# Performance work log

Hardware: AMD Instinct MI355X
Metric: run time of the kernel (lower is better)

Reference implementation:

```python
import jax, jax.numpy as jnp
import numpy as np

LN_EPS = 1e-6

def _ln_proj(x, ln_scale, ln_bias, kernel, bias):
    # LayerNorm over last dim, then GEMM projection. Dropout is identity
    # (deterministic / eval mode, training=False default).
    mu = jnp.mean(x, axis=-1, keepdims=True)
    var = jnp.mean(jnp.square(x - mu), axis=-1, keepdims=True)
    xn = (x - mu) * jax.lax.rsqrt(var + LN_EPS) * ln_scale + ln_bias
    return jnp.einsum('bsh,hp->bsp', xn, kernel) + bias


def setup_inputs() -> dict:
    key = jax.random.key(0)
    ks = jax.random.split(key, 4)
    B, S, H, P = 2, 4096, 4096, 1024
    return {
        'vision_features': jax.random.normal(ks[0], (B, S, H), dtype=jnp.float32),
        'text_features': jax.random.normal(ks[1], (B, S, H), dtype=jnp.float32),
        'v_ln_scale': jnp.ones((H,), jnp.float32),
        'v_ln_bias': jnp.zeros((H,), jnp.float32),
        'v_kernel': jax.random.normal(ks[2], (H, P), dtype=jnp.float32) / np.sqrt(H).astype(np.float32),
        'v_bias': jnp.zeros((P,), jnp.float32),
        't_ln_scale': jnp.ones((H,), jnp.float32),
        't_ln_bias': jnp.zeros((H,), jnp.float32),
        't_kernel': jax.random.normal(ks[3], (H, P), dtype=jnp.float32) / np.sqrt(H).astype(np.float32),
        't_bias': jnp.zeros((P,), jnp.float32),
    }


def reference(vision_features, text_features, v_ln_scale, v_ln_bias, v_kernel, v_bias,
              t_ln_scale, t_ln_bias, t_kernel, t_bias):
    vision_projected = _ln_proj(vision_features, v_ln_scale, v_ln_bias, v_kernel, v_bias)
    text_projected = _ln_proj(text_features, t_ln_scale, t_ln_bias, t_kernel, t_bias)
    return (vision_projected, text_projected)
```

## Files before the change

### kernel.cpp

```cpp
#include <hip/hip_runtime.h>
#include <hip/hip_bf16.h>
#include <stdint.h>

#define LN_EPS 1e-6f

typedef __bf16 bf16x8 __attribute__((ext_vector_type(8)));
typedef float f32x4 __attribute__((ext_vector_type(4)));

__device__ __forceinline__ unsigned short f2bf(float f) {
    uint32_t u = __float_as_uint(f);
    uint32_t r = (u + 0x7fffu + ((u >> 16) & 1u)) >> 16;
    return (unsigned short)r;
}

__device__ __forceinline__ void async_copy16(const void* g, void* l) {
    const __attribute__((address_space(1))) uint32_t* gp =
        (const __attribute__((address_space(1))) uint32_t*)(uintptr_t)g;
    __attribute__((address_space(3))) uint32_t* lp =
        (__attribute__((address_space(3))) uint32_t*)(uint32_t)(uintptr_t)l;
    __builtin_amdgcn_global_load_lds(gp, lp, 16, 0, 0);
}

__global__ __launch_bounds__(256) void ln_bf16_kernel(
    const float* __restrict__ x0, const float* __restrict__ x1,
    const float* __restrict__ s0, const float* __restrict__ b0,
    const float* __restrict__ s1, const float* __restrict__ b1,
    unsigned short* __restrict__ y0, unsigned short* __restrict__ y1, int H)
{
    int row = blockIdx.x;
    int prob = blockIdx.y;
    const float* x = (prob ? x1 : x0) + (size_t)row * H;
    const float* s = prob ? s1 : s0;
    const float* b = prob ? b1 : b0;
    unsigned short* y = (prob ? y1 : y0) + (size_t)row * H;
    int t = threadIdx.x;

    float4 v[4];
    float sum = 0.f, sq = 0.f;
#pragma unroll
    for (int g = 0; g < 4; ++g) {
        v[g] = ((const float4*)x)[t + 256 * g];
        sum += v[g].x + v[g].y + v[g].z + v[g].w;
        sq  += v[g].x * v[g].x + v[g].y * v[g].y + v[g].z * v[g].z + v[g].w * v[g].w;
    }
#pragma unroll
    for (int off = 32; off > 0; off >>= 1) {
        sum += __shfl_xor(sum, off, 64);
        sq  += __shfl_xor(sq, off, 64);
    }
    __shared__ float ssum[4], ssq[4];
    int wave = t >> 6;
    if ((t & 63) == 0) { ssum[wave] = sum; ssq[wave] = sq; }
    __syncthreads();
    sum = ssum[0] + ssum[1] + ssum[2] + ssum[3];
    sq  = ssq[0] + ssq[1] + ssq[2] + ssq[3];
    float mu = sum * (1.0f / 4096.0f);
    float var = sq * (1.0f / 4096.0f) - mu * mu;
    float rstd = rsqrtf(var + LN_EPS);

#pragma unroll
    for (int g = 0; g < 4; ++g) {
        int i4 = t + 256 * g;
        float4 sc = ((const float4*)s)[i4];
        float4 bi = ((const float4*)b)[i4];
        ushort4 o;
        o.x = f2bf((v[g].x - mu) * rstd * sc.x + bi.x);
        o.y = f2bf((v[g].y - mu) * rstd * sc.y + bi.y);
        o.z = f2bf((v[g].z - mu) * rstd * sc.z + bi.z);
        o.w = f2bf((v[g].w - mu) * rstd * sc.w + bi.w);
        ((ushort4*)y)[i4] = o;
    }
}

__global__ __launch_bounds__(256) void cast_transpose_kernel(
    const float* __restrict__ w0, const float* __restrict__ w1,
    unsigned short* __restrict__ o0, unsigned short* __restrict__ o1,
    int K, int N)
{
    int prob = blockIdx.z;
    const float* w = prob ? w1 : w0;
    unsigned short* o = prob ? o1 : o0;
    __shared__ unsigned short tile[32][33];
    int tx = threadIdx.x & 31;
    int ty = threadIdx.x >> 5;
    int n0 = blockIdx.x * 32;
    int k0 = blockIdx.y * 32;
#pragma unroll
    for (int i = 0; i < 4; ++i) {
        int k = ty + 8 * i;
        tile[k][tx] = f2bf(w[(size_t)(k0 + k) * N + n0 + tx]);
    }
    __syncthreads();
#pragma unroll
    for (int i = 0; i < 4; ++i) {
        int n = ty + 8 * i;
        o[(size_t)(n0 + n) * K + k0 + tx] = tile[tx][n];
    }
}

#define BM 128
#define BN 128
#define BK 32

__global__ __launch_bounds__(256) void gemm_bf16_kernel(
    const unsigned short* __restrict__ A0, const unsigned short* __restrict__ A1,
    const unsigned short* __restrict__ W0, const unsigned short* __restrict__ W1,
    const float* __restrict__ bias0, const float* __restrict__ bias1,
    float* __restrict__ out0, float* __restrict__ out1,
    int M, int N, int K)
{
    int prob = blockIdx.z;
    const unsigned short* A = prob ? A1 : A0;
    const unsigned short* W = prob ? W1 : W0;
    const float* bias = prob ? bias1 : bias0;
    float* out = prob ? out1 : out0;

    __shared__ unsigned short As[BM * BK];
    __shared__ unsigned short Bs[BN * BK];

    int t = threadIdx.x;
    int wave = t >> 6, lane = t & 63;
    int quad = lane >> 4, r16 = lane & 15;
    int wm = wave >> 1, wn = wave & 1;

    int tile_m = blockIdx.y * BM;
    int tile_n = blockIdx.x * BN;

    f32x4 acc[4][4] = {};

    for (int k0 = 0; k0 < K; k0 += BK) {
#pragma unroll
        for (int q = 0; q < 2; ++q) {
            int c = wave * 128 + q * 64 + lane;
            int row = c >> 2, kb = c & 3;
            const unsigned short* ga = A + (size_t)(tile_m + row) * K + k0 + kb * 8;
            const unsigned short* gb = W + (size_t)(tile_n + row) * K + k0 + kb * 8;
            uint32_t lbase = (uint32_t)(wave * 128 + q * 64) * 16;
            async_copy16(ga, (char*)As + lbase);
            async_copy16(gb, (char*)Bs + lbase);
        }
        __syncthreads();

        bf16x8 af[4], bfr[4];
#pragma unroll
        for (int i = 0; i < 4; ++i) {
            af[i]  = *(const bf16x8*)((const char*)As + (wm * 64 + i * 16 + r16) * 64 + quad * 16);
            bfr[i] = *(const bf16x8*)((const char*)Bs + (wn * 64 + i * 16 + r16) * 64 + quad * 16);
        }
#pragma unroll
        for (int i = 0; i < 4; ++i)
#pragma unroll
            for (int j = 0; j < 4; ++j)
                acc[i][j] = __builtin_amdgcn_mfma_f32_16x16x32_bf16(af[i], bfr[j], acc[i][j], 0, 0, 0);
        __syncthreads();
    }

#pragma unroll
    for (int j = 0; j < 4; ++j) {
        int col = tile_n + wn * 64 + j * 16 + r16;
        float bj = bias[col];
#pragma unroll
        for (int i = 0; i < 4; ++i) {
            int row = tile_m + wm * 64 + i * 16 + quad * 4;
#pragma unroll
            for (int r = 0; r < 4; ++r)
                out[(size_t)(row + r) * N + col] = acc[i][j][r] + bj;
        }
    }
}

extern "C" void kernel_launch(void* const* d_in, const int* in_sizes, int n_in,
                              void* d_out, int out_size, void* d_ws, size_t ws_size,
                              hipStream_t stream) {
    const float* xv = (const float*)d_in[0];
    const float* xt = (const float*)d_in[1];
    const float* sv = (const float*)d_in[2];
    const float* bv = (const float*)d_in[3];
    const float* wv = (const float*)d_in[4];
    const float* biasv = (const float*)d_in[5];
    const float* st = (const float*)d_in[6];
    const float* bt = (const float*)d_in[7];
    const float* wt = (const float*)d_in[8];
    const float* biast = (const float*)d_in[9];
    float* out = (float*)d_out;

    const int B = 2, S = 4096, H = 4096, P = 1024;
    const int M = B * S;
    float* outv = out;
    float* outt = out + (size_t)M * P;

    size_t xnBytes = (size_t)M * H * 2;
    size_t wtBytes = (size_t)P * H * 2;
    char* ws = (char*)d_ws;

    if (ws_size >= 2 * xnBytes + 2 * wtBytes) {
        unsigned short* Xv = (unsigned short*)(ws);
        unsigned short* Xt = (unsigned short*)(ws + xnBytes);
        unsigned short* Wv = (unsigned short*)(ws + 2 * xnBytes);
        unsigned short* Wt = (unsigned short*)(ws + 2 * xnBytes + wtBytes);
        ln_bf16_kernel<<<dim3(M, 2), 256, 0, stream>>>(xv, xt, sv, bv, st, bt, Xv, Xt, H);
        cast_transpose_kernel<<<dim3(P / 32, H / 32, 2), 256, 0, stream>>>(wv, wt, Wv, Wt, H, P);
        gemm_bf16_kernel<<<dim3(P / BN, M / BM, 2), 256, 0, stream>>>(
            Xv, Xt, Wv, Wt, biasv, biast, outv, outt, M, P, H);
    } else {
        unsigned short* X  = (unsigned short*)(ws);
        unsigned short* Wb = (unsigned short*)(ws + xnBytes);
        ln_bf16_kernel<<<dim3(M, 1), 256, 0, stream>>>(xv, xv, sv, bv, sv, bv, X, X, H);
        cast_transpose_kernel<<<dim3(P / 32, H / 32, 1), 256, 0, stream>>>(wv, wv, Wb, Wb, H, P);
        gemm_bf16_kernel<<<dim3(P / BN, M / BM, 1), 256, 0, stream>>>(
            X, X, Wb, Wb, biasv, biasv, outv, outv, M, P, H);
        ln_bf16_kernel<<<dim3(M, 1), 256, 0, stream>>>(xt, xt, st, bt, st, bt, X, X, H);
        cast_transpose_kernel<<<dim3(P / 32, H / 32, 1), 256, 0, stream>>>(wt, wt, Wb, Wb, H, P);
        gemm_bf16_kernel<<<dim3(P / BN, M / BM, 1), 256, 0, stream>>>(
            X, X, Wb, Wb, biast, biast, outt, outt, M, P, H);
    }
}
```

Measured before the change: 583.9 us.

## Double GEMM K-tile and remap blocks to XCDs for L2 locality

Measured after the change: 555.2 us. 1.05x faster.

```diff
diff --git a/kernel.cpp b/kernel.cpp
--- a/kernel.cpp
+++ b/kernel.cpp
@@ -100,7 +100,7 @@
 
 #define BM 128
 #define BN 128
-#define BK 32
+#define BK 64
 
 __global__ __launch_bounds__(256) void gemm_bf16_kernel(
     const unsigned short* __restrict__ A0, const unsigned short* __restrict__ A1,
@@ -109,7 +109,14 @@
     float* __restrict__ out0, float* __restrict__ out1,
     int M, int N, int K)
 {
-    int prob = blockIdx.z;
+    int id = blockIdx.x;
+    int xcd = id & 7;
+    int l = id >> 3;
+    int prob = l >> 6;
+    int rem = l & 63;
+    int mt = xcd * 8 + (rem >> 3);
+    int nt = rem & 7;
+
     const unsigned short* A = prob ? A1 : A0;
     const unsigned short* W = prob ? W1 : W0;
     const float* bias = prob ? bias1 : bias0;
@@ -123,35 +130,46 @@
     int quad = lane >> 4, r16 = lane & 15;
     int wm = wave >> 1, wn = wave & 1;
 
-    int tile_m = blockIdx.y * BM;
-    int tile_n = blockIdx.x * BN;
+    int tile_m = mt * BM;
+    int tile_n = nt * BN;
+
+    int c = t;
+    const unsigned short* ga[4];
+    const unsigned short* gb[4];
+#pragma unroll
+    for (int q = 0; q < 4; ++q) {
+        int cc = q * 256 + t;
+        int row = cc >> 3, kb = cc & 7;
+        ga[q] = A + (size_t)(tile_m + row) * K + kb * 8;
+        gb[q] = W + (size_t)(tile_n + row) * K + kb * 8;
+    }
+    (void)c;
 
     f32x4 acc[4][4] = {};
 
     for (int k0 = 0; k0 < K; k0 += BK) {
 #pragma unroll
-        for (int q = 0; q < 2; ++q) {
-            int c = wave * 128 + q * 64 + lane;
-            int row = c >> 2, kb = c & 3;
-            const unsigned short* ga = A + (size_t)(tile_m + row) * K + k0 + kb * 8;
-            const unsigned short* gb = W + (size_t)(tile_n + row) * K + k0 + kb * 8;
-            uint32_t lbase = (uint32_t)(wave * 128 + q * 64) * 16;
-            async_copy16(ga, (char*)As + lbase);
-            async_copy16(gb, (char*)Bs + lbase);
+        for (int q = 0; q < 4; ++q) {
+            uint32_t lbase = (uint32_t)(q * 256 + wave * 64) * 16;
+            async_copy16(ga[q] + k0, (char*)As + lbase);
+            async_copy16(gb[q] + k0, (char*)Bs + lbase);
         }
         __syncthreads();
 
-        bf16x8 af[4], bfr[4];
-#pragma unroll
-        for (int i = 0; i < 4; ++i) {
-            af[i]  = *(const bf16x8*)((const char*)As + (wm * 64 + i * 16 + r16) * 64 + quad * 16);
-            bfr[i] = *(const bf16x8*)((const char*)Bs + (wn * 64 + i * 16 + r16) * 64 + quad * 16);
+#pragma unroll
+        for (int s = 0; s < 2; ++s) {
+            bf16x8 af[4], bfr[4];
+#pragma unroll
+            for (int i = 0; i < 4; ++i) {
+                af[i]  = *(const bf16x8*)(As + (wm * 64 + i * 16 + r16) * 64 + (s * 4 + quad) * 8);
+                bfr[i] = *(const bf16x8*)(Bs + (wn * 64 + i * 16 + r16) * 64 + (s * 4 + quad) * 8);
+            }
+#pragma unroll
+            for (int i = 0; i < 4; ++i)
+#pragma unroll
+                for (int j = 0; j < 4; ++j)
+                    acc[i][j] = __builtin_amdgcn_mfma_f32_16x16x32_bf16(af[i], bfr[j], acc[i][j], 0, 0, 0);
         }
-#pragma unroll
-        for (int i = 0; i < 4; ++i)
-#pragma unroll
-            for (int j = 0; j < 4; ++j)
-                acc[i][j] = __builtin_amdgcn_mfma_f32_16x16x32_bf16(af[i], bfr[j], acc[i][j], 0, 0, 0);
         __syncthreads();
     }
 
@@ -200,18 +218,18 @@
         unsigned short* Wt = (unsigned short*)(ws + 2 * xnBytes + wtBytes);
         ln_bf16_kernel<<<dim3(M, 2), 256, 0, stream>>>(xv, xt, sv, bv, st, bt, Xv, Xt, H);
         cast_transpose_kernel<<<dim3(P / 32, H / 32, 2), 256, 0, stream>>>(wv, wt, Wv, Wt, H, P);
-        gemm_bf16_kernel<<<dim3(P / BN, M / BM, 2), 256, 0, stream>>>(
+        gemm_bf16_kernel<<<dim3(1024), 256, 0, stream>>>(
             Xv, Xt, Wv, Wt, biasv, biast, outv, outt, M, P, H);
     } else {
         unsigned short* X  = (unsigned short*)(ws);
         unsigned short* Wb = (unsigned short*)(ws + xnBytes);
         ln_bf16_kernel<<<dim3(M, 1), 256, 0, stream>>>(xv, xv, sv, bv, sv, bv, X, X, H);
         cast_transpose_kernel<<<dim3(P / 32, H / 32, 1), 256, 0, stream>>>(wv, wv, Wb, Wb, H, P);
-        gemm_bf16_kernel<<<dim3(P / BN, M / BM, 1), 256, 0, stream>>>(
+        gemm_bf16_kernel<<<dim3(512), 256, 0, stream>>>(
             X, X, Wb, Wb, biasv, biasv, outv, outv, M, P, H);
         ln_bf16_kernel<<<dim3(M, 1), 256, 0, stream>>>(xt, xt, st, bt, st, bt, X, X, H);
         cast_transpose_kernel<<<dim3(P / 32, H / 32, 1), 256, 0, stream>>>(wt, wt, Wb, Wb, H, P);
-        gemm_bf16_kernel<<<dim3(P / BN, M / BM, 1), 256, 0, stream>>>(
+        gemm_bf16_kernel<<<dim3(512), 256, 0, stream>>>(
             X, X, Wb, Wb, biast, biast, outt, outt, M, P, H);
     }
 }
```
